# Kernel optimization log

Measured on AMD Instinct MI355X. Metric: run time of the kernel, lower is better.

Reference implementation:

```python
import jax, jax.numpy as jnp
import numpy as np

N = 200000      # nodes per graph batch side
E = 3200000     # edges per side (avg degree 16)
NG = 1000       # number of graphs per side
CIN = 64
F1, F2, F3, D = 64, 32, 16, 16
BN_EPS = 1e-5


def gin_conv(x, edge_index, eps, W1, b1, W2, b2, gamma, beta):
    # GINConv: nn((1+eps)*x + sum_{j->i} x_j), nn = Lin-ReLU-Lin-BatchNorm1d (batch stats)
    src, dst = edge_index[0], edge_index[1]
    agg = jax.ops.segment_sum(x[src], dst, num_segments=x.shape[0])
    h = (1.0 + eps) * x + agg
    h = jax.nn.relu(h @ W1 + b1) @ W2 + b2
    mu = jnp.mean(h, axis=0)
    var = jnp.var(h, axis=0)
    return gamma * (h - mu) * jax.lax.rsqrt(var + BN_EPS) + beta


def global_attention_readout(x, batch, W, b):
    # global_mean_pool -> sigmoid fc -> gated global_add_pool
    ones = jnp.ones((x.shape[0], 1), x.dtype)
    cnt = jax.ops.segment_sum(ones, batch, num_segments=NG)
    summ = jax.ops.segment_sum(x, batch, num_segments=NG)
    mean = summ / jnp.maximum(cnt, 1.0)
    c = jax.nn.sigmoid(mean @ W + b)          # [NG, F3]
    c_n = c[batch]                             # broadcast back to nodes
    gate = jax.nn.sigmoid(jnp.sum(x * c_n, axis=1, keepdims=True))
    return jax.ops.segment_sum(gate * x, batch, num_segments=NG)


def efn(h_i, h_j, aW1, ab1, aW2, ab2, mW, mb):
    h = jnp.concatenate([h_i, h_j], axis=1)   # [NG, 2*F3]
    att = jnp.tanh(jax.nn.relu(h @ aW1 + ab1) @ aW2 + ab2)
    enc = att * h + h
    return jax.nn.relu(enc @ mW + mb)         # [NG, D]


def setup_inputs() -> dict:
    key = jax.random.key(0)
    ks = iter(jax.random.split(key, 48))
    def nrm(shape, s=0.1):
        return jax.random.normal(next(ks), shape, jnp.float32) * s
    inp = {}
    inp["x_i"] = jax.random.normal(next(ks), (N, CIN), jnp.float32)
    inp["x_j"] = jax.random.normal(next(ks), (N, CIN), jnp.float32)
    inp["edge_index_i"] = jax.random.randint(next(ks), (2, E), 0, N, dtype=jnp.int32)
    inp["edge_index_j"] = jax.random.randint(next(ks), (2, E), 0, N, dtype=jnp.int32)
    inp["batch_i"] = jnp.sort(jax.random.randint(next(ks), (N,), 0, NG, dtype=jnp.int32))
    inp["batch_j"] = jnp.sort(jax.random.randint(next(ks), (N,), 0, NG, dtype=jnp.int32))
    # GINConv 1 (train_eps=True, init 0)
    inp["eps1"] = jnp.zeros((), jnp.float32)
    inp["g1_W1"], inp["g1_b1"] = nrm((CIN, F1)), jnp.zeros((F1,), jnp.float32)
    inp["g1_W2"], inp["g1_b2"] = nrm((F1, F1)), jnp.zeros((F1,), jnp.float32)
    inp["g1_g"], inp["g1_bt"] = jnp.ones((F1,), jnp.float32), jnp.zeros((F1,), jnp.float32)
    inp["eps2"] = jnp.zeros((), jnp.float32)
    inp["g2_W1"], inp["g2_b1"] = nrm((F1, F2)), jnp.zeros((F2,), jnp.float32)
    inp["g2_W2"], inp["g2_b2"] = nrm((F2, F2)), jnp.zeros((F2,), jnp.float32)
    inp["g2_g"], inp["g2_bt"] = jnp.ones((F2,), jnp.float32), jnp.zeros((F2,), jnp.float32)
    inp["eps3"] = jnp.zeros((), jnp.float32)
    inp["g3_W1"], inp["g3_b1"] = nrm((F2, F3)), jnp.zeros((F3,), jnp.float32)
    inp["g3_W2"], inp["g3_b2"] = nrm((F3, F3)), jnp.zeros((F3,), jnp.float32)
    inp["g3_g"], inp["g3_bt"] = jnp.ones((F3,), jnp.float32), jnp.zeros((F3,), jnp.float32)
    # global attention fc
    inp["att_W"], inp["att_b"] = nrm((F3, F3)), jnp.zeros((F3,), jnp.float32)
    # EFN: in=2*F3=32, reduction=4 -> 8
    inp["efn_aW1"], inp["efn_ab1"] = nrm((2 * F3, 8)), jnp.zeros((8,), jnp.float32)
    inp["efn_aW2"], inp["efn_ab2"] = nrm((8, 2 * F3)), jnp.zeros((2 * F3,), jnp.float32)
    inp["efn_mW"], inp["efn_mb"] = nrm((2 * F3, D)), jnp.zeros((D,), jnp.float32)
    # final fc: D -> D//2 -> 1
    inp["fc_W1"], inp["fc_b1"] = nrm((D, D // 2)), jnp.zeros((D // 2,), jnp.float32)
    inp["fc_W2"], inp["fc_b2"] = nrm((D // 2, 1)), jnp.zeros((1,), jnp.float32)
    return inp


def reference(x_i, x_j, edge_index_i, edge_index_j, batch_i, batch_j,
              eps1, g1_W1, g1_b1, g1_W2, g1_b2, g1_g, g1_bt,
              eps2, g2_W1, g2_b1, g2_W2, g2_b2, g2_g, g2_bt,
              eps3, g3_W1, g3_b1, g3_W2, g3_b2, g3_g, g3_bt,
              att_W, att_b,
              efn_aW1, efn_ab1, efn_aW2, efn_ab2, efn_mW, efn_mb,
              fc_W1, fc_b1, fc_W2, fc_b2):
    xi1 = gin_conv(x_i, edge_index_i, eps1, g1_W1, g1_b1, g1_W2, g1_b2, g1_g, g1_bt)
    xj1 = gin_conv(x_j, edge_index_j, eps1, g1_W1, g1_b1, g1_W2, g1_b2, g1_g, g1_bt)
    xi2 = gin_conv(xi1, edge_index_i, eps2, g2_W1, g2_b1, g2_W2, g2_b2, g2_g, g2_bt)
    xj2 = gin_conv(xj1, edge_index_j, eps2, g2_W1, g2_b1, g2_W2, g2_b2, g2_g, g2_bt)
    xi3 = gin_conv(xi2, edge_index_i, eps3, g3_W1, g3_b1, g3_W2, g3_b2, g3_g, g3_bt)
    xj3 = gin_conv(xj2, edge_index_j, eps3, g3_W1, g3_b1, g3_W2, g3_b2, g3_g, g3_bt)
    h_i = global_attention_readout(xi3, batch_i, att_W, att_b)
    h_j = global_attention_readout(xj3, batch_j, att_W, att_b)
    h_AB = efn(h_i, h_j, efn_aW1, efn_ab1, efn_aW2, efn_ab2, efn_mW, efn_mb)
    h_AA = efn(h_i, h_i, efn_aW1, efn_ab1, efn_aW2, efn_ab2, efn_mW, efn_mb)
    h_BB = efn(h_j, h_j, efn_aW1, efn_ab1, efn_aW2, efn_ab2, efn_mW, efn_mb)
    h_Ab = h_AB - h_BB
    h_aB = h_AB - h_AA
    score = (jax.nn.relu(h_AB @ fc_W1 + fc_b1) @ fc_W2 + fc_b2).squeeze(1)
    return (score, h_Ab, h_aB)
```

## Files before the change

### kernel.cpp

```cpp
#include <hip/hip_runtime.h>
#include <math.h>

#define NGRAPH 1000
#define BKSHIFT 11
#define BKMASK 2047
#define NBK_MAX 128
#define PART_BLOCKS 256
#define LCAP 33792

typedef unsigned short ushort_t;
typedef __attribute__((ext_vector_type(8))) short short8;
typedef __attribute__((ext_vector_type(8))) _Float16 half8;
typedef __attribute__((ext_vector_type(4))) float floatx4;

static __device__ inline ushort_t f2bf(float f) {
  unsigned u = __float_as_uint(f);
  u = (u + 0x7fffu + ((u >> 16) & 1u)) >> 16;
  return (ushort_t)u;
}
static __device__ inline ushort_t f2h_bits(float f) {
  return __builtin_bit_cast(ushort_t, (_Float16)f);
}
static __device__ inline float h2f_bits(ushort_t u) {
  return (float)__builtin_bit_cast(_Float16, u);
}


__global__ __launch_bounds__(1024) void bucket_hist2(const int* __restrict__ dst0,
                                                     const int* __restrict__ dst1, int E,
                                                     int chunk, int* __restrict__ hist, int nbk) {
  const int side = blockIdx.y;
  const int* __restrict__ dst = side ? dst1 : dst0;
  __shared__ int lh[NBK_MAX];
  for (int i = threadIdx.x; i < nbk; i += 1024) lh[i] = 0;
  __syncthreads();
  const int e0 = blockIdx.x * chunk;
  const int e1 = min(E, e0 + chunk);
  for (int e = e0 + threadIdx.x; e < e1; e += 1024) atomicAdd(&lh[dst[e] >> BKSHIFT], 1);
  __syncthreads();
  int* row = hist + ((size_t)side * PART_BLOCKS + blockIdx.x) * nbk;
  for (int i = threadIdx.x; i < nbk; i += 1024) row[i] = lh[i];
}

__global__ __launch_bounds__(PART_BLOCKS) void colscan_par2(int* __restrict__ hist, int nbk,
                                                            int* __restrict__ totals) {
  __shared__ int s[PART_BLOCKS];
  const int side = blockIdx.y;
  int* __restrict__ hist_s = hist + (size_t)side * PART_BLOCKS * nbk;
  int* __restrict__ totals_s = totals + side * nbk;
  const int b = blockIdx.x;
  const int t = threadIdx.x;
  s[t] = hist_s[(size_t)t * nbk + b];
  __syncthreads();
  for (int off = 1; off < PART_BLOCKS; off <<= 1) {
    int u = (t >= off) ? s[t - off] : 0;
    __syncthreads();
    s[t] += u;
    __syncthreads();
  }
  const int exc = (t == 0) ? 0 : s[t - 1];
  hist_s[(size_t)t * nbk + b] = exc;
  if (t == PART_BLOCKS - 1) totals_s[b] = s[PART_BLOCKS - 1];
}

__global__ __launch_bounds__(1024) void scan_small2(const int* __restrict__ in, int n,
                                                    int* __restrict__ out) {
  __shared__ int s[2048];
  const int side = blockIdx.x;
  const int* __restrict__ in_s = in + side * n;
  int* __restrict__ out_s = out + side * (n + 1);
  const int t = threadIdx.x;
  s[t] = (t < n) ? in_s[t] : 0;
  s[t + 1024] = (t + 1024 < n) ? in_s[t + 1024] : 0;
  __syncthreads();
  for (int off = 1; off < 2048; off <<= 1) {
    int v0 = (t >= off) ? s[t - off] : 0;
    int v1 = ((t + 1024) >= off) ? s[t + 1024 - off] : 0;
    __syncthreads();
    s[t] += v0;
    s[t + 1024] += v1;
    __syncthreads();
  }
  if (t < n) out_s[t] = (t == 0) ? 0 : s[t - 1];
  const int u = t + 1024;
  if (u < n) out_s[u] = s[u - 1];
  if (t == 0) out_s[n] = s[n - 1];
}

__global__ __launch_bounds__(1024) void partition2(const int* __restrict__ src0,
                                                   const int* __restrict__ src1,
                                                   const int* __restrict__ dst0,
                                                   const int* __restrict__ dst1, int E, int chunk,
                                                   const int* __restrict__ hist,
                                                   const int* __restrict__ boff,
                                                   unsigned* __restrict__ ebufA,
                                                   unsigned* __restrict__ ebufB, int nbk) {
  const int side = blockIdx.y;
  const int* __restrict__ src = side ? src1 : src0;
  const int* __restrict__ dst = side ? dst1 : dst0;
  const int* __restrict__ boff_s = boff + side * (nbk + 1);
  unsigned* __restrict__ ebuf = side ? ebufB : ebufA;
  __shared__ int lbase[NBK_MAX];
  __shared__ int lcur[NBK_MAX];
  const int* row = hist + ((size_t)side * PART_BLOCKS + blockIdx.x) * nbk;
  for (int i = threadIdx.x; i < nbk; i += 1024) {
    lbase[i] = boff_s[i] + row[i];
    lcur[i] = 0;
  }
  __syncthreads();
  const int e0 = blockIdx.x * chunk;
  const int e1 = min(E, e0 + chunk);
  for (int e = e0 + threadIdx.x; e < e1; e += 1024) {
    int d = dst[e];
    int b = d >> BKSHIFT;
    int pos = lbase[b] + atomicAdd(&lcur[b], 1);
    ebuf[pos] = ((unsigned)src[e] << BKSHIFT) | (unsigned)(d & BKMASK);
  }
}

__global__ __launch_bounds__(1024) void bucket_csr2(const unsigned* __restrict__ ebufA,
                                                    const unsigned* __restrict__ ebufB,
                                                    const int* __restrict__ boff,
                                                    int* __restrict__ row_ptrA,
                                                    int* __restrict__ colA,
                                                    int* __restrict__ row_ptrB,
                                                    int* __restrict__ colB, int N, int E,
                                                    int nbk) {
  __shared__ int cnt[2048];
  __shared__ int lcol[LCAP];
  const int side = blockIdx.y;
  const unsigned* __restrict__ ebuf = side ? ebufB : ebufA;
  const int* __restrict__ boff_s = boff + side * (nbk + 1);
  int* __restrict__ row_ptr = side ? row_ptrB : row_ptrA;
  int* __restrict__ col = side ? colB : colA;
  const int b = blockIdx.x;
  const int node0 = b << BKSHIFT;
  const int nn = min(2048, N - node0);
  const int es = boff_s[b], ee = boff_s[b + 1];
  const int ne = ee - es;
  const int t = threadIdx.x;
  cnt[t] = 0;
  cnt[t + 1024] = 0;
  __syncthreads();
  for (int e = es + t; e < ee; e += 1024) atomicAdd(&cnt[ebuf[e] & (unsigned)BKMASK], 1);
  __syncthreads();
  for (int off = 1; off < 2048; off <<= 1) {
    int v0 = (t >= off) ? cnt[t - off] : 0;
    int v1 = ((t + 1024) >= off) ? cnt[t + 1024 - off] : 0;
    __syncthreads();
    cnt[t] += v0;
    cnt[t + 1024] += v1;
    __syncthreads();
  }
  const int ex0 = (t == 0) ? 0 : cnt[t - 1];
  const int ex1 = cnt[t + 1023];
  if (t < nn) row_ptr[node0 + t] = es + ex0;
  if (t + 1024 < nn) row_ptr[node0 + t + 1024] = es + ex1;
  __syncthreads();
  cnt[t] = ex0;
  cnt[t + 1024] = ex1;
  __syncthreads();
  if (ne <= LCAP) {
    for (int e = es + t; e < ee; e += 1024) {
      unsigned u = ebuf[e];
      int li = (int)(u & (unsigned)BKMASK);
      int pos = atomicAdd(&cnt[li], 1);
      lcol[pos] = (int)(u >> BKSHIFT);
    }
    __syncthreads();
    for (int i = t; i < ne; i += 1024) col[es + i] = lcol[i];
  } else {
    for (int e = es + t; e < ee; e += 1024) {
      unsigned u = ebuf[e];
      int li = (int)(u & (unsigned)BKMASK);
      int pos = es + atomicAdd(&cnt[li], 1);
      col[pos] = (int)(u >> BKSHIFT);
    }
  }
  if (b == 0 && t == 0) row_ptr[N] = E;
}


template <int FIN, int FOUT, bool HAS_BN, bool IN_HALF>
__global__ __launch_bounds__(256) void lin_mfma(const void* __restrict__ xin,
                                                const float* __restrict__ W,
                                                const float* __restrict__ stats,
                                                const float* __restrict__ gamma,
                                                const float* __restrict__ beta, float invN,
                                                ushort_t* __restrict__ y, int n) {
  constexpr int KC = FIN / 32;
  constexpr int FT = FOUT / 16;
  __shared__ _Float16 Whf[FIN * FOUT];
  __shared__ float scv[FIN], ofv[FIN];
  const int tid = threadIdx.x;
  for (int i = tid; i < FIN * FOUT; i += 256) Whf[i] = (_Float16)W[i];
  for (int i = tid; i < FIN; i += 256) {
    if constexpr (HAS_BN) {
      float mu = stats[i] * invN;
      float var = stats[128 + i] * invN - mu * mu;
      float s = gamma[i] * rsqrtf(var + 1e-5f);
      scv[i] = s;
      ofv[i] = beta[i] - s * mu;
    } else {
      scv[i] = 1.f;
      ofv[i] = 0.f;
    }
  }
  __syncthreads();
  const int lane = tid & 63, wv = tid >> 6;
  const int colf = lane & 15, quad = lane >> 4, kbase = quad * 8;

  half8 Bf[FT][KC];
#pragma unroll
  for (int t = 0; t < FT; t++)
#pragma unroll
    for (int c = 0; c < KC; c++)
#pragma unroll
      for (int j = 0; j < 8; j++)
        Bf[t][c][j] = Whf[(c * 32 + kbase + j) * FOUT + t * 16 + colf];

  const floatx4 zero4 = {0.f, 0.f, 0.f, 0.f};
  const int ntiles = (n + 15) >> 4;
  for (int nt = blockIdx.x * 4 + wv; nt < ntiles; nt += gridDim.x * 4) {
    const int node0 = nt << 4;
    const int anode = node0 + colf;
    half8 Af[KC];
#pragma unroll
    for (int c = 0; c < KC; c++) {
      if (anode < n) {
        const int kk = c * 32 + kbase;
        if constexpr (IN_HALF) {
          const ushort_t* hp = (const ushort_t*)xin + (size_t)anode * FIN + kk;
          half8 hv = *(const half8*)hp;
#pragma unroll
          for (int j = 0; j < 8; j++)
            Af[c][j] = (_Float16)fmaf((float)hv[j], scv[kk + j], ofv[kk + j]);
        } else {
          const float* xp = (const float*)xin + (size_t)anode * FIN + kk;
          float4 xa = *(const float4*)xp;
          float4 xb = *(const float4*)(xp + 4);
          Af[c][0] = (_Float16)fmaf(xa.x, scv[kk + 0], ofv[kk + 0]);
          Af[c][1] = (_Float16)fmaf(xa.y, scv[kk + 1], ofv[kk + 1]);
          Af[c][2] = (_Float16)fmaf(xa.z, scv[kk + 2], ofv[kk + 2]);
          Af[c][3] = (_Float16)fmaf(xa.w, scv[kk + 3], ofv[kk + 3]);
          Af[c][4] = (_Float16)fmaf(xb.x, scv[kk + 4], ofv[kk + 4]);
          Af[c][5] = (_Float16)fmaf(xb.y, scv[kk + 5], ofv[kk + 5]);
          Af[c][6] = (_Float16)fmaf(xb.z, scv[kk + 6], ofv[kk + 6]);
          Af[c][7] = (_Float16)fmaf(xb.w, scv[kk + 7], ofv[kk + 7]);
        }
      } else {
        Af[c] = half8{0, 0, 0, 0, 0, 0, 0, 0};
      }
    }
#pragma unroll
    for (int t = 0; t < FT; t++) {
      floatx4 acc = zero4;
#pragma unroll
      for (int c = 0; c < KC; c++)
        acc = __builtin_amdgcn_mfma_f32_16x16x32_f16(Af[c], Bf[t][c], acc, 0, 0, 0);
#pragma unroll
      for (int r = 0; r < 4; r++) {
        const int row = node0 + quad * 4 + r;
        if (row < n) y[(size_t)row * FOUT + t * 16 + colf] = f2bf(acc[r]);
      }
    }
  }
}


template <int F>
__global__ __launch_bounds__(256) void lin2s_mfma(const ushort_t* __restrict__ m,
                                                  const float* __restrict__ W,
                                                  const float* __restrict__ b,
                                                  ushort_t* __restrict__ h,
                                                  float* __restrict__ stats, int n) {
  constexpr int KC = (F + 31) / 32;
  constexpr int FT = F / 16;
  __shared__ ushort_t Wbf[F * F];
  __shared__ float bs[F], ls[F], lsq[F];
  const int tid = threadIdx.x;
  for (int i = tid; i < F * F; i += 256) Wbf[i] = f2bf(W[i]);
  if (tid < F) {
    bs[tid] = b[tid];
    ls[tid] = 0.f;
    lsq[tid] = 0.f;
  }
  __syncthreads();
  const int lane = tid & 63, wv = tid >> 6;
  const int colf = lane & 15, quad = lane >> 4, kbase = quad * 8;

  short8 Bf[FT][KC];
#pragma unroll
  for (int t = 0; t < FT; t++)
#pragma unroll
    for (int c = 0; c < KC; c++)
#pragma unroll
      for (int j = 0; j < 8; j++) {
        const int k = c * 32 + kbase + j;
        Bf[t][c][j] = (k < F) ? (short)Wbf[k * F + t * 16 + colf] : (short)0;
      }

  const floatx4 zero4 = {0.f, 0.f, 0.f, 0.f};
  float ssum[FT], ssq[FT];
#pragma unroll
  for (int t = 0; t < FT; t++) {
    ssum[t] = 0.f;
    ssq[t] = 0.f;
  }

  const int ntiles = (n + 15) >> 4;
  for (int nt = blockIdx.x * 4 + wv; nt < ntiles; nt += gridDim.x * 4) {
    const int node0 = nt << 4;
    const int anode = node0 + colf;
    short8 Af[KC];
#pragma unroll
    for (int c = 0; c < KC; c++) {
      const int kk = c * 32 + kbase;
      if (anode < n && kk < F)
        Af[c] = *(const short8*)(m + (size_t)anode * F + kk);
      else
        Af[c] = short8{0, 0, 0, 0, 0, 0, 0, 0};
    }
#pragma unroll
    for (int t = 0; t < FT; t++) {
      floatx4 acc = zero4;
#pragma unroll
      for (int c = 0; c < KC; c++)
        acc = __builtin_amdgcn_mfma_f32_16x16x32_bf16(Af[c], Bf[t][c], acc, 0, 0, 0);
      const float bv = bs[t * 16 + colf];
#pragma unroll
      for (int r = 0; r < 4; r++) {
        const int row = node0 + quad * 4 + r;
        if (row < n) {
          float o = acc[r] + bv;
          h[(size_t)row * F + t * 16 + colf] = f2h_bits(o);
          ssum[t] += o;
          ssq[t] += o * o;
        }
      }
    }
  }
#pragma unroll
  for (int t = 0; t < FT; t++) {
    atomicAdd(&ls[t * 16 + colf], ssum[t]);
    atomicAdd(&lsq[t * 16 + colf], ssq[t]);
  }
  __syncthreads();
  if (tid < F) {
    atomicAdd(&stats[tid], ls[tid]);
    atomicAdd(&stats[128 + tid], lsq[tid]);
  }
}


template <int F>
__global__ __launch_bounds__(256) void aggrelu_b(const ushort_t* __restrict__ y,
                                                 const int* __restrict__ row_ptr,
                                                 const int* __restrict__ col,
                                                 const float* __restrict__ epsp,
                                                 const float* __restrict__ b1,
                                                 ushort_t* __restrict__ m, int n) {
  constexpr int LPN = F / 8;
  constexpr int NPB = 256 / LPN;
  const int tid = threadIdx.x;
  const int ln = tid / LPN;
  const int fl = tid % LPN;
  const float e1 = 1.0f + epsp[0];
  const float4 b1a = ((const float4*)b1)[fl * 2];
  const float4 b1b = ((const float4*)b1)[fl * 2 + 1];

  const int node = blockIdx.x * NPB + ln;
  if (node >= n) return;
  const uint4* yr = (const uint4*)y;
  const size_t rowi = (size_t)node * LPN + fl;
  const int rs = row_ptr[node], re = row_ptr[node + 1];

  float acc[8];
#pragma unroll
  for (int j = 0; j < 8; j++) acc[j] = 0.f;

  auto addv = [&](uint4 v) {
    acc[0] += __uint_as_float(v.x << 16);
    acc[1] += __uint_as_float(v.x & 0xffff0000u);
    acc[2] += __uint_as_float(v.y << 16);
    acc[3] += __uint_as_float(v.y & 0xffff0000u);
    acc[4] += __uint_as_float(v.z << 16);
    acc[5] += __uint_as_float(v.z & 0xffff0000u);
    acc[6] += __uint_as_float(v.w << 16);
    acc[7] += __uint_as_float(v.w & 0xffff0000u);
  };

  int e = rs;
  for (; e + 8 <= re; e += 8) {
    int c0 = col[e], c1 = col[e + 1], c2 = col[e + 2], c3 = col[e + 3];
    int c4 = col[e + 4], c5 = col[e + 5], c6 = col[e + 6], c7 = col[e + 7];
    uint4 v0 = yr[(size_t)c0 * LPN + fl];
    uint4 v1 = yr[(size_t)c1 * LPN + fl];
    uint4 v2 = yr[(size_t)c2 * LPN + fl];
    uint4 v3 = yr[(size_t)c3 * LPN + fl];
    uint4 v4 = yr[(size_t)c4 * LPN + fl];
    uint4 v5 = yr[(size_t)c5 * LPN + fl];
    uint4 v6 = yr[(size_t)c6 * LPN + fl];
    uint4 v7 = yr[(size_t)c7 * LPN + fl];
    addv(v0);
    addv(v1);
    addv(v2);
    addv(v3);
    addv(v4);
    addv(v5);
    addv(v6);
    addv(v7);
  }
  for (; e + 4 <= re; e += 4) {
    int c0 = col[e], c1 = col[e + 1], c2 = col[e + 2], c3 = col[e + 3];
    uint4 v0 = yr[(size_t)c0 * LPN + fl];
    uint4 v1 = yr[(size_t)c1 * LPN + fl];
    uint4 v2 = yr[(size_t)c2 * LPN + fl];
    uint4 v3 = yr[(size_t)c3 * LPN + fl];
    addv(v0);
    addv(v1);
    addv(v2);
    addv(v3);
  }
  for (; e < re; e++) addv(yr[(size_t)col[e] * LPN + fl]);

  uint4 sv = yr[rowi];
  float r0, r1, r2, r3, r4, r5, r6, r7;
  r0 = fmaxf(fmaf(e1, __uint_as_float(sv.x << 16), acc[0]) + b1a.x, 0.f);
  r1 = fmaxf(fmaf(e1, __uint_as_float(sv.x & 0xffff0000u), acc[1]) + b1a.y, 0.f);
  r2 = fmaxf(fmaf(e1, __uint_as_float(sv.y << 16), acc[2]) + b1a.z, 0.f);
  r3 = fmaxf(fmaf(e1, __uint_as_float(sv.y & 0xffff0000u), acc[3]) + b1a.w, 0.f);
  r4 = fmaxf(fmaf(e1, __uint_as_float(sv.z << 16), acc[4]) + b1b.x, 0.f);
  r5 = fmaxf(fmaf(e1, __uint_as_float(sv.z & 0xffff0000u), acc[5]) + b1b.y, 0.f);
  r6 = fmaxf(fmaf(e1, __uint_as_float(sv.w << 16), acc[6]) + b1b.z, 0.f);
  r7 = fmaxf(fmaf(e1, __uint_as_float(sv.w & 0xffff0000u), acc[7]) + b1b.w, 0.f);
  uint4 o;
  o.x = (unsigned)f2bf(r0) | ((unsigned)f2bf(r1) << 16);
  o.y = (unsigned)f2bf(r2) | ((unsigned)f2bf(r3) << 16);
  o.z = (unsigned)f2bf(r4) | ((unsigned)f2bf(r5) << 16);
  o.w = (unsigned)f2bf(r6) | ((unsigned)f2bf(r7) << 16);
  ((uint4*)m)[rowi] = o;
}


__global__ __launch_bounds__(256) void readout_fused(
    const ushort_t* __restrict__ h3, const int* __restrict__ batch, int n,
    const float* __restrict__ stats, const float* __restrict__ gamma,
    const float* __restrict__ beta, float invN, const float* __restrict__ attW,
    const float* __restrict__ attb, float* __restrict__ hg, int ng) {
  __shared__ float sM[16], oM[16], red[16][17], meanM[16], cM[16];
  __shared__ int seg[2];
  const int tid = threadIdx.x;
  const int g = blockIdx.x;
  const int f = tid & 15, slot = tid >> 4;
  if (tid < 16) {
    float mu = stats[tid] * invN;
    float var = stats[128 + tid] * invN - mu * mu;
    float s = gamma[tid] * rsqrtf(var + 1e-5f);
    sM[tid] = s;
    oM[tid] = beta[tid] - s * mu;
  }
  if (tid >= 32 && tid < 34) {
    const int key = g + (tid - 32);
    int lo = 0, hi = n;
    while (lo < hi) {
      int mid = (lo + hi) >> 1;
      if (batch[mid] < key) lo = mid + 1; else hi = mid;
    }
    seg[tid - 32] = lo;
  }
  __syncthreads();
  const int s0 = seg[0], e0 = seg[1];
  const float sf = sM[f], of = oM[f];

  float acc = 0.f;
  for (int node = s0 + slot; node < e0; node += 16)
    acc += fmaf(h2f_bits(h3[(size_t)node * 16 + f]), sf, of);
  red[slot][f] = acc;
  __syncthreads();
  if (tid < 16) {
    float t = 0.f;
    for (int s = 0; s < 16; s++) t += red[s][tid];
    meanM[tid] = t / fmaxf((float)(e0 - s0), 1.f);
  }
  __syncthreads();
  if (tid < 16) {
    float a = attb[tid];
    for (int k = 0; k < 16; k++) a += meanM[k] * attW[k * 16 + tid];
    cM[tid] = 1.f / (1.f + expf(-a));
  }
  __syncthreads();
  const float cf = cM[f];
  float acc2 = 0.f;
  for (int node = s0 + slot; node < e0; node += 16) {
    float xv = fmaf(h2f_bits(h3[(size_t)node * 16 + f]), sf, of);
    float p = xv * cf;
    for (int m = 8; m >= 1; m >>= 1) p += __shfl_xor(p, m, 16);
    acc2 += xv / (1.f + expf(-p));
  }
  red[slot][f] = acc2;
  __syncthreads();
  if (tid < 16) {
    float t = 0.f;
    for (int s = 0; s < 16; s++) t += red[s][tid];
    hg[g * 16 + tid] = t;
  }
}


__global__ __launch_bounds__(256) void final3_kernel(
    const float* __restrict__ hgA, const float* __restrict__ hgB, const float* __restrict__ aW1,
    const float* __restrict__ ab1, const float* __restrict__ aW2, const float* __restrict__ ab2,
    const float* __restrict__ mW, const float* __restrict__ mb, const float* __restrict__ fcW1,
    const float* __restrict__ fcb1, const float* __restrict__ fcW2,
    const float* __restrict__ fcb2, float* __restrict__ out, int ng) {
  __shared__ float aW1s[256], aW2s[256], mWs[512], fcW1s[128];
  __shared__ float ab1s[8], ab2s[32], mbs[16], fcb1s[8], fcW2s[8];
  __shared__ float fcb2s;
  __shared__ float hb[16][33], m8b[16][9], encb[16][33], abb[16][17], tb[16][9];
  const int tid = threadIdx.x;
  aW1s[tid] = aW1[tid];
  aW2s[tid] = aW2[tid];
  mWs[tid] = mW[tid];
  mWs[256 + tid] = mW[256 + tid];
  if (tid < 128) fcW1s[tid] = fcW1[tid];
  if (tid < 8) {
    ab1s[tid] = ab1[tid];
    fcb1s[tid] = fcb1[tid];
    fcW2s[tid] = fcW2[tid];
  }
  if (tid < 32) ab2s[tid] = ab2[tid];
  if (tid < 16) mbs[tid] = mb[tid];
  if (tid == 0) fcb2s = fcb2[0];
  __syncthreads();

  const int g = tid >> 4;
  const int l = tid & 15;
  const int gg = blockIdx.x * 16 + g;
  const bool valid = gg < ng;
  const float hiv = valid ? hgA[gg * 16 + l] : 0.f;
  const float hjv = valid ? hgB[gg * 16 + l] : 0.f;
  float res[3];

#pragma unroll
  for (int p = 0; p < 3; p++) {
    float ha = (p == 2) ? hjv : hiv;
    float h2 = (p == 1) ? hiv : hjv;
    hb[g][l] = ha;
    hb[g][16 + l] = h2;
    __syncthreads();
    if (l < 8) {
      float t = ab1s[l];
#pragma unroll
      for (int k = 0; k < 32; k++) t += hb[g][k] * aW1s[k * 8 + l];
      m8b[g][l] = fmaxf(t, 0.f);
    }
    __syncthreads();
    float e0 = ab2s[l], e1 = ab2s[16 + l];
#pragma unroll
    for (int k = 0; k < 8; k++) {
      float mv = m8b[g][k];
      e0 += mv * aW2s[k * 32 + l];
      e1 += mv * aW2s[k * 32 + 16 + l];
    }
    float a0 = tanhf(e0), a1 = tanhf(e1);
    encb[g][l] = fmaf(a0, ha, ha);
    encb[g][16 + l] = fmaf(a1, h2, h2);
    __syncthreads();
    float o = mbs[l];
#pragma unroll
    for (int k = 0; k < 32; k++) o += encb[g][k] * mWs[k * 16 + l];
    res[p] = fmaxf(o, 0.f);
    __syncthreads();
  }

  if (valid) {
    out[ng + gg * 16 + l] = res[0] - res[2];
    out[ng + ng * 16 + gg * 16 + l] = res[0] - res[1];
  }
  abb[g][l] = res[0];
  __syncthreads();
  if (l < 8) {
    float t = fcb1s[l];
#pragma unroll
    for (int k = 0; k < 16; k++) t += abb[g][k] * fcW1s[k * 8 + l];
    tb[g][l] = fmaxf(t, 0.f);
  }
  __syncthreads();
  if (l == 0 && valid) {
    float sc = fcb2s;
#pragma unroll
    for (int o = 0; o < 8; o++) sc += tb[g][o] * fcW2s[o];
    out[gg] = sc;
  }
}


extern "C" void kernel_launch(void* const* d_in, const int* in_sizes, int n_in, void* d_out,
                              int out_size, void* d_ws, size_t ws_size, hipStream_t stream) {
  (void)n_in;
  (void)out_size;
  (void)ws_size;
  const int N = in_sizes[0] / 64;
  const int E = in_sizes[2] / 2;
  const int NG = NGRAPH;
  const int NBK = (N + BKMASK) >> BKSHIFT;
  const int CHUNK = (E + PART_BLOCKS - 1) / PART_BLOCKS;

  char* w = (char*)d_ws;
  auto alloc = [&](size_t bytes) -> void* {
    void* p = (void*)w;
    w += (bytes + 255) & ~(size_t)255;
    return p;
  };
  int* row_ptrA = (int*)alloc((size_t)(N + 1) * 4);
  int* colA = (int*)alloc((size_t)E * 4);
  int* row_ptrB = (int*)alloc((size_t)(N + 1) * 4);
  int* colB = (int*)alloc((size_t)E * 4);
  int* hist = (int*)alloc((size_t)2 * PART_BLOCKS * NBK * 4);
  int* totals = (int*)alloc((size_t)2 * NBK * 4);
  int* boff = (int*)alloc((size_t)2 * (NBK + 1) * 4);
  ushort_t* bufA = (ushort_t*)alloc((size_t)N * 64 * 2);
  ushort_t* bufB = (ushort_t*)alloc((size_t)N * 64 * 2);
  float* stats = (float*)alloc((size_t)2 * 768 * 4);
  float* hgA = (float*)alloc((size_t)NG * 16 * 4);
  float* hgB = (float*)alloc((size_t)NG * 16 * 4);

  unsigned* ebufA = (unsigned*)bufA;
  unsigned* ebufB = ebufA + E;
  ushort_t* y1 = bufB;
  ushort_t* m1 = bufA;
  ushort_t* h1 = bufB;
  ushort_t* y2 = bufA;
  ushort_t* m2 = bufA + (size_t)N * 32;
  ushort_t* h2 = bufB;
  ushort_t* y3 = bufA;
  ushort_t* m3 = bufA + (size_t)N * 16;
  ushort_t* h3 = bufB;

  const int* esrc0 = (const int*)d_in[2];
  const int* edst0 = esrc0 + E;
  const int* esrc1 = (const int*)d_in[3];
  const int* edst1 = esrc1 + E;
  const float* attW = (const float*)d_in[27];
  const float* attb = (const float*)d_in[28];
  const float invN = 1.0f / (float)N;

  bucket_hist2<<<dim3(PART_BLOCKS, 2), 1024, 0, stream>>>(edst0, edst1, E, CHUNK, hist, NBK);
  colscan_par2<<<dim3(NBK, 2), PART_BLOCKS, 0, stream>>>(hist, NBK, totals);
  scan_small2<<<2, 1024, 0, stream>>>(totals, NBK, boff);
  partition2<<<dim3(PART_BLOCKS, 2), 1024, 0, stream>>>(esrc0, esrc1, edst0, edst1, E, CHUNK,
                                                        hist, boff, ebufA, ebufB, NBK);
  bucket_csr2<<<dim3(NBK, 2), 1024, 0, stream>>>(ebufA, ebufB, boff, row_ptrA, colA, row_ptrB,
                                                 colB, N, E, NBK);
  hipMemsetAsync(stats, 0, 2 * 768 * 4, stream);

  for (int s = 0; s < 2; s++) {
    const float* x0 = (const float*)d_in[s];
    const int* batch = (const int*)d_in[4 + s];
    const int* row_ptr = s ? row_ptrB : row_ptrA;
    const int* col = s ? colB : colA;
    float* st = stats + s * 768;
    float* hg = s ? hgB : hgA;

    lin_mfma<64, 64, false, false><<<512, 256, 0, stream>>>(
        x0, (const float*)d_in[7], nullptr, nullptr, nullptr, invN, y1, N);
    aggrelu_b<64><<<(N + 31) / 32, 256, 0, stream>>>(
        y1, row_ptr, col, (const float*)d_in[6], (const float*)d_in[8], m1, N);
    lin2s_mfma<64><<<512, 256, 0, stream>>>(m1, (const float*)d_in[9], (const float*)d_in[10],
                                            h1, st, N);

    lin_mfma<64, 32, true, true><<<512, 256, 0, stream>>>(
        h1, (const float*)d_in[14], st, (const float*)d_in[11], (const float*)d_in[12], invN,
        y2, N);
    aggrelu_b<32><<<(N + 63) / 64, 256, 0, stream>>>(
        y2, row_ptr, col, (const float*)d_in[13], (const float*)d_in[15], m2, N);
    lin2s_mfma<32><<<512, 256, 0, stream>>>(m2, (const float*)d_in[16], (const float*)d_in[17],
                                            h2, st + 256, N);

    lin_mfma<32, 16, true, true><<<512, 256, 0, stream>>>(
        h2, (const float*)d_in[21], st + 256, (const float*)d_in[18], (const float*)d_in[19],
        invN, y3, N);
    aggrelu_b<16><<<(N + 127) / 128, 256, 0, stream>>>(
        y3, row_ptr, col, (const float*)d_in[20], (const float*)d_in[22], m3, N);
    lin2s_mfma<16><<<512, 256, 0, stream>>>(m3, (const float*)d_in[23], (const float*)d_in[24],
                                            h3, st + 512, N);

    readout_fused<<<NG, 256, 0, stream>>>(h3, batch, N, st + 512, (const float*)d_in[25],
                                          (const float*)d_in[26], invN, attW, attb, hg, NG);
  }

  final3_kernel<<<(NG + 15) / 16, 256, 0, stream>>>(
      hgA, hgB, (const float*)d_in[29], (const float*)d_in[30], (const float*)d_in[31],
      (const float*)d_in[32], (const float*)d_in[33], (const float*)d_in[34],
      (const float*)d_in[35], (const float*)d_in[36], (const float*)d_in[37],
      (const float*)d_in[38], (float*)d_out, NG);
}
```

Baseline: 827.7 us.

## Batch both graph sides into single launches via blockIdx.y

Merges the per-side loop so each GIN stage (linear, aggregation, second linear with stats, readout) runs once over both graph sides, with blockIdx.y selecting the side's buffers. Per-side scratch buffers are doubled so both sides can be live at once. This halves the number of kernel launches and doubles the grid per launch, which helps fill the GPU in small kernels like readout and cuts launch gaps. The cost is twice the scratch memory and a larger working set per kernel, which may lower cache hit rates in the gather.

```diff
diff --git a/kernel.cpp b/kernel.cpp
--- a/kernel.cpp
+++ b/kernel.cpp
@@ -182,14 +182,21 @@
 
 
 template <int FIN, int FOUT, bool HAS_BN, bool IN_HALF>
-__global__ __launch_bounds__(256) void lin_mfma(const void* __restrict__ xin,
-                                                const float* __restrict__ W,
-                                                const float* __restrict__ stats,
-                                                const float* __restrict__ gamma,
-                                                const float* __restrict__ beta, float invN,
-                                                ushort_t* __restrict__ y, int n) {
+__global__ __launch_bounds__(256) void lin_mfma2(const void* __restrict__ xin0,
+                                                 const void* __restrict__ xin1,
+                                                 const float* __restrict__ W,
+                                                 const float* __restrict__ st0,
+                                                 const float* __restrict__ st1,
+                                                 const float* __restrict__ gamma,
+                                                 const float* __restrict__ beta, float invN,
+                                                 ushort_t* __restrict__ y0,
+                                                 ushort_t* __restrict__ y1, int n) {
   constexpr int KC = FIN / 32;
   constexpr int FT = FOUT / 16;
+  const int side = blockIdx.y;
+  const void* __restrict__ xin = side ? xin1 : xin0;
+  const float* __restrict__ stats = side ? st1 : st0;
+  ushort_t* __restrict__ y = side ? y1 : y0;
   __shared__ _Float16 Whf[FIN * FOUT];
   __shared__ float scv[FIN], ofv[FIN];
   const int tid = threadIdx.x;
@@ -269,13 +276,20 @@
 
 
 template <int F>
-__global__ __launch_bounds__(256) void lin2s_mfma(const ushort_t* __restrict__ m,
-                                                  const float* __restrict__ W,
-                                                  const float* __restrict__ b,
-                                                  ushort_t* __restrict__ h,
-                                                  float* __restrict__ stats, int n) {
+__global__ __launch_bounds__(256) void lin2s_mfma2(const ushort_t* __restrict__ m0,
+                                                   const ushort_t* __restrict__ m1,
+                                                   const float* __restrict__ W,
+                                                   const float* __restrict__ b,
+                                                   ushort_t* __restrict__ h0,
+                                                   ushort_t* __restrict__ h1,
+                                                   float* __restrict__ st0,
+                                                   float* __restrict__ st1, int n) {
   constexpr int KC = (F + 31) / 32;
   constexpr int FT = F / 16;
+  const int side = blockIdx.y;
+  const ushort_t* __restrict__ m = side ? m1 : m0;
+  ushort_t* __restrict__ h = side ? h1 : h0;
+  float* __restrict__ stats = side ? st1 : st0;
   __shared__ ushort_t Wbf[F * F];
   __shared__ float bs[F], ls[F], lsq[F];
   const int tid = threadIdx.x;
@@ -354,14 +368,23 @@
 
 
 template <int F>
-__global__ __launch_bounds__(256) void aggrelu_b(const ushort_t* __restrict__ y,
-                                                 const int* __restrict__ row_ptr,
-                                                 const int* __restrict__ col,
-                                                 const float* __restrict__ epsp,
-                                                 const float* __restrict__ b1,
-                                                 ushort_t* __restrict__ m, int n) {
+__global__ __launch_bounds__(256) void aggrelu_b2(const ushort_t* __restrict__ ya,
+                                                  const ushort_t* __restrict__ yb,
+                                                  const int* __restrict__ rp0,
+                                                  const int* __restrict__ rp1,
+                                                  const int* __restrict__ c0,
+                                                  const int* __restrict__ c1,
+                                                  const float* __restrict__ epsp,
+                                                  const float* __restrict__ b1,
+                                                  ushort_t* __restrict__ ma,
+                                                  ushort_t* __restrict__ mb, int n) {
   constexpr int LPN = F / 8;
   constexpr int NPB = 256 / LPN;
+  const int side = blockIdx.y;
+  const ushort_t* __restrict__ y = side ? yb : ya;
+  const int* __restrict__ row_ptr = side ? rp1 : rp0;
+  const int* __restrict__ col = side ? c1 : c0;
+  ushort_t* __restrict__ m = side ? mb : ma;
   const int tid = threadIdx.x;
   const int ln = tid / LPN;
   const int fl = tid % LPN;
@@ -392,16 +415,16 @@
 
   int e = rs;
   for (; e + 8 <= re; e += 8) {
-    int c0 = col[e], c1 = col[e + 1], c2 = col[e + 2], c3 = col[e + 3];
-    int c4 = col[e + 4], c5 = col[e + 5], c6 = col[e + 6], c7 = col[e + 7];
-    uint4 v0 = yr[(size_t)c0 * LPN + fl];
-    uint4 v1 = yr[(size_t)c1 * LPN + fl];
-    uint4 v2 = yr[(size_t)c2 * LPN + fl];
-    uint4 v3 = yr[(size_t)c3 * LPN + fl];
-    uint4 v4 = yr[(size_t)c4 * LPN + fl];
-    uint4 v5 = yr[(size_t)c5 * LPN + fl];
-    uint4 v6 = yr[(size_t)c6 * LPN + fl];
-    uint4 v7 = yr[(size_t)c7 * LPN + fl];
+    int d0 = col[e], d1 = col[e + 1], d2 = col[e + 2], d3 = col[e + 3];
+    int d4 = col[e + 4], d5 = col[e + 5], d6 = col[e + 6], d7 = col[e + 7];
+    uint4 v0 = yr[(size_t)d0 * LPN + fl];
+    uint4 v1 = yr[(size_t)d1 * LPN + fl];
+    uint4 v2 = yr[(size_t)d2 * LPN + fl];
+    uint4 v3 = yr[(size_t)d3 * LPN + fl];
+    uint4 v4 = yr[(size_t)d4 * LPN + fl];
+    uint4 v5 = yr[(size_t)d5 * LPN + fl];
+    uint4 v6 = yr[(size_t)d6 * LPN + fl];
+    uint4 v7 = yr[(size_t)d7 * LPN + fl];
     addv(v0);
     addv(v1);
     addv(v2);
@@ -412,11 +435,11 @@
     addv(v7);
   }
   for (; e + 4 <= re; e += 4) {
-    int c0 = col[e], c1 = col[e + 1], c2 = col[e + 2], c3 = col[e + 3];
-    uint4 v0 = yr[(size_t)c0 * LPN + fl];
-    uint4 v1 = yr[(size_t)c1 * LPN + fl];
-    uint4 v2 = yr[(size_t)c2 * LPN + fl];
-    uint4 v3 = yr[(size_t)c3 * LPN + fl];
+    int d0 = col[e], d1 = col[e + 1], d2 = col[e + 2], d3 = col[e + 3];
+    uint4 v0 = yr[(size_t)d0 * LPN + fl];
+    uint4 v1 = yr[(size_t)d1 * LPN + fl];
+    uint4 v2 = yr[(size_t)d2 * LPN + fl];
+    uint4 v3 = yr[(size_t)d3 * LPN + fl];
     addv(v0);
     addv(v1);
     addv(v2);
@@ -443,13 +466,20 @@
 }
 
 
-__global__ __launch_bounds__(256) void readout_fused(
-    const ushort_t* __restrict__ h3, const int* __restrict__ batch, int n,
-    const float* __restrict__ stats, const float* __restrict__ gamma,
-    const float* __restrict__ beta, float invN, const float* __restrict__ attW,
-    const float* __restrict__ attb, float* __restrict__ hg, int ng) {
+__global__ __launch_bounds__(256) void readout_fused2(
+    const ushort_t* __restrict__ h3a, const ushort_t* __restrict__ h3b,
+    const int* __restrict__ batch0, const int* __restrict__ batch1, int n,
+    const float* __restrict__ st0, const float* __restrict__ st1,
+    const float* __restrict__ gamma, const float* __restrict__ beta, float invN,
+    const float* __restrict__ attW, const float* __restrict__ attb,
+    float* __restrict__ hgA, float* __restrict__ hgB, int ng) {
   __shared__ float sM[16], oM[16], red[16][17], meanM[16], cM[16];
   __shared__ int seg[2];
+  const int side = blockIdx.y;
+  const ushort_t* __restrict__ h3 = side ? h3b : h3a;
+  const int* __restrict__ batch = side ? batch1 : batch0;
+  const float* __restrict__ stats = side ? st1 : st0;
+  float* __restrict__ hg = side ? hgB : hgA;
   const int tid = threadIdx.x;
   const int g = blockIdx.x;
   const int f = tid & 15, slot = tid >> 4;
@@ -620,28 +650,23 @@
   int* hist = (int*)alloc((size_t)2 * PART_BLOCKS * NBK * 4);
   int* totals = (int*)alloc((size_t)2 * NBK * 4);
   int* boff = (int*)alloc((size_t)2 * (NBK + 1) * 4);
-  ushort_t* bufA = (ushort_t*)alloc((size_t)N * 64 * 2);
-  ushort_t* bufB = (ushort_t*)alloc((size_t)N * 64 * 2);
+  ushort_t* sA = (ushort_t*)alloc((size_t)2 * N * 64 * 2);
+  ushort_t* sB = (ushort_t*)alloc((size_t)2 * N * 64 * 2);
   float* stats = (float*)alloc((size_t)2 * 768 * 4);
   float* hgA = (float*)alloc((size_t)NG * 16 * 4);
   float* hgB = (float*)alloc((size_t)NG * 16 * 4);
 
-  unsigned* ebufA = (unsigned*)bufA;
-  unsigned* ebufB = ebufA + E;
-  ushort_t* y1 = bufB;
-  ushort_t* m1 = bufA;
-  ushort_t* h1 = bufB;
-  ushort_t* y2 = bufA;
-  ushort_t* m2 = bufA + (size_t)N * 32;
-  ushort_t* h2 = bufB;
-  ushort_t* y3 = bufA;
-  ushort_t* m3 = bufA + (size_t)N * 16;
-  ushort_t* h3 = bufB;
+  ushort_t* bA[2] = {sA, sA + (size_t)N * 64};
+  ushort_t* bB[2] = {sB, sB + (size_t)N * 64};
+  unsigned* ebuf0 = (unsigned*)bA[0];
+  unsigned* ebuf1 = (unsigned*)bA[1];
 
   const int* esrc0 = (const int*)d_in[2];
   const int* edst0 = esrc0 + E;
   const int* esrc1 = (const int*)d_in[3];
   const int* edst1 = esrc1 + E;
+  const int* batch0 = (const int*)d_in[4];
+  const int* batch1 = (const int*)d_in[5];
   const float* attW = (const float*)d_in[27];
   const float* attb = (const float*)d_in[28];
   const float invN = 1.0f / (float)N;
@@ -650,45 +675,47 @@
   colscan_par2<<<dim3(NBK, 2), PART_BLOCKS, 0, stream>>>(hist, NBK, totals);
   scan_small2<<<2, 1024, 0, stream>>>(totals, NBK, boff);
   partition2<<<dim3(PART_BLOCKS, 2), 1024, 0, stream>>>(esrc0, esrc1, edst0, edst1, E, CHUNK,
-                                                        hist, boff, ebufA, ebufB, NBK);
-  bucket_csr2<<<dim3(NBK, 2), 1024, 0, stream>>>(ebufA, ebufB, boff, row_ptrA, colA, row_ptrB,
+                                                        hist, boff, ebuf0, ebuf1, NBK);
+  bucket_csr2<<<dim3(NBK, 2), 1024, 0, stream>>>(ebuf0, ebuf1, boff, row_ptrA, colA, row_ptrB,
                                                  colB, N, E, NBK);
   hipMemsetAsync(stats, 0, 2 * 768 * 4, stream);
 
-  for (int s = 0; s < 2; s++) {
-    const float* x0 = (const float*)d_in[s];
-    const int* batch = (const int*)d_in[4 + s];
-    const int* row_ptr = s ? row_ptrB : row_ptrA;
-    const int* col = s ? colB : colA;
-    float* st = stats + s * 768;
-    float* hg = s ? hgB : hgA;
-
-    lin_mfma<64, 64, false, false><<<512, 256, 0, stream>>>(
-        x0, (const float*)d_in[7], nullptr, nullptr, nullptr, invN, y1, N);
-    aggrelu_b<64><<<(N + 31) / 32, 256, 0, stream>>>(
-        y1, row_ptr, col, (const float*)d_in[6], (const float*)d_in[8], m1, N);
-    lin2s_mfma<64><<<512, 256, 0, stream>>>(m1, (const float*)d_in[9], (const float*)d_in[10],
-                                            h1, st, N);
-
-    lin_mfma<64, 32, true, true><<<512, 256, 0, stream>>>(
-        h1, (const float*)d_in[14], st, (const float*)d_in[11], (const float*)d_in[12], invN,
-        y2, N);
-    aggrelu_b<32><<<(N + 63) / 64, 256, 0, stream>>>(
-        y2, row_ptr, col, (const float*)d_in[13], (const float*)d_in[15], m2, N);
-    lin2s_mfma<32><<<512, 256, 0, stream>>>(m2, (const float*)d_in[16], (const float*)d_in[17],
-                                            h2, st + 256, N);
-
-    lin_mfma<32, 16, true, true><<<512, 256, 0, stream>>>(
-        h2, (const float*)d_in[21], st + 256, (const float*)d_in[18], (const float*)d_in[19],
-        invN, y3, N);
-    aggrelu_b<16><<<(N + 127) / 128, 256, 0, stream>>>(
-        y3, row_ptr, col, (const float*)d_in[20], (const float*)d_in[22], m3, N);
-    lin2s_mfma<16><<<512, 256, 0, stream>>>(m3, (const float*)d_in[23], (const float*)d_in[24],
-                                            h3, st + 512, N);
-
-    readout_fused<<<NG, 256, 0, stream>>>(h3, batch, N, st + 512, (const float*)d_in[25],
-                                          (const float*)d_in[26], invN, attW, attb, hg, NG);
-  }
+  float* st0 = stats;
+  float* st1 = stats + 768;
+
+  lin_mfma2<64, 64, false, false><<<dim3(512, 2), 256, 0, stream>>>(
+      d_in[0], d_in[1], (const float*)d_in[7], nullptr, nullptr, nullptr, nullptr, invN,
+      bB[0], bB[1], N);
+  aggrelu_b2<64><<<dim3((N + 31) / 32, 2), 256, 0, stream>>>(
+      bB[0], bB[1], row_ptrA, row_ptrB, colA, colB, (const float*)d_in[6],
+      (const float*)d_in[8], bA[0], bA[1], N);
+  lin2s_mfma2<64><<<dim3(512, 2), 256, 0, stream>>>(bA[0], bA[1], (const float*)d_in[9],
+                                                    (const float*)d_in[10], bB[0], bB[1],
+                                                    st0, st1, N);
+
+  lin_mfma2<64, 32, true, true><<<dim3(512, 2), 256, 0, stream>>>(
+      bB[0], bB[1], (const float*)d_in[14], st0, st1, (const float*)d_in[11],
+      (const float*)d_in[12], invN, bA[0], bA[1], N);
+  aggrelu_b2<32><<<dim3((N + 63) / 64, 2), 256, 0, stream>>>(
+      bA[0], bA[1], row_ptrA, row_ptrB, colA, colB, (const float*)d_in[13],
+      (const float*)d_in[15], bA[0] + (size_t)N * 32, bA[1] + (size_t)N * 32, N);
+  lin2s_mfma2<32><<<dim3(512, 2), 256, 0, stream>>>(
+      bA[0] + (size_t)N * 32, bA[1] + (size_t)N * 32, (const float*)d_in[16],
+      (const float*)d_in[17], bB[0], bB[1], st0 + 256, st1 + 256, N);
+
+  lin_mfma2<32, 16, true, true><<<dim3(512, 2), 256, 0, stream>>>(
+      bB[0], bB[1], (const float*)d_in[21], st0 + 256, st1 + 256, (const float*)d_in[18],
+      (const float*)d_in[19], invN, bA[0], bA[1], N);
+  aggrelu_b2<16><<<dim3((N + 127) / 128, 2), 256, 0, stream>>>(
+      bA[0], bA[1], row_ptrA, row_ptrB, colA, colB, (const float*)d_in[20],
+      (const float*)d_in[22], bA[0] + (size_t)N * 16, bA[1] + (size_t)N * 16, N);
+  lin2s_mfma2<16><<<dim3(512, 2), 256, 0, stream>>>(
+      bA[0] + (size_t)N * 16, bA[1] + (size_t)N * 16, (const float*)d_in[23],
+      (const float*)d_in[24], bB[0], bB[1], st0 + 512, st1 + 512, N);
+
+  readout_fused2<<<dim3(NG, 2), 256, 0, stream>>>(
+      bB[0], bB[1], batch0, batch1, N, st0 + 512, st1 + 512, (const float*)d_in[25],
+      (const float*)d_in[26], invN, attW, attb, hgA, hgB, NG);
 
   final3_kernel<<<(NG + 15) / 16, 256, 0, stream>>>(
       hgA, hgB, (const float*)d_in[29], (const float*)d_in[30], (const float*)d_in[31],
```

New measurement: 738.3 us, median of 2. -10.8%, faster.
